# Performance work log

Measured on AMD Instinct MI355X. Metric: run time of the kernel, lower is better.

The kernel has to match this reference:

```python
import jax, jax.numpy as jnp
import numpy as np

EMBED_DIM = 1024
NUM_HEADS = 16
HEAD_DIM = EMBED_DIM // NUM_HEADS
B, S = 4, 2048


def setup_inputs() -> dict:
    key = jax.random.key(0)
    ks = jax.random.split(key, 9)
    scale = 1.0 / np.sqrt(EMBED_DIM)
    x = jax.random.normal(ks[0], (B, S, EMBED_DIM), dtype=jnp.float32)
    Wq = jax.random.uniform(ks[1], (EMBED_DIM, EMBED_DIM), jnp.float32, -scale, scale)
    bq = jax.random.uniform(ks[2], (EMBED_DIM,), jnp.float32, -scale, scale)
    Wk = jax.random.uniform(ks[3], (EMBED_DIM, EMBED_DIM), jnp.float32, -scale, scale)
    bk = jax.random.uniform(ks[4], (EMBED_DIM,), jnp.float32, -scale, scale)
    Wv = jax.random.uniform(ks[5], (EMBED_DIM, EMBED_DIM), jnp.float32, -scale, scale)
    bv = jax.random.uniform(ks[6], (EMBED_DIM,), jnp.float32, -scale, scale)
    Wo = jax.random.uniform(ks[7], (EMBED_DIM, EMBED_DIM), jnp.float32, -scale, scale)
    bo = jax.random.uniform(ks[8], (EMBED_DIM,), jnp.float32, -scale, scale)
    return {"x": x, "Wq": Wq, "bq": bq, "Wk": Wk, "bk": bk, "Wv": Wv, "bv": bv, "Wo": Wo, "bo": bo}


def reference(x, Wq, bq, Wk, bk, Wv, bv, Wo, bo):
    b, s, d = x.shape
    h, hd = NUM_HEADS, HEAD_DIM
    # projections -> [b, h, s, hd]
    def proj(W, bias):
        return (x @ W + bias).reshape(b, s, h, hd).transpose(0, 2, 1, 3)
    q = proj(Wq, bq)
    k = proj(Wk, bk)
    v = proj(Wv, bv)
    logits = jnp.einsum('bhqd,bhkd->bhqk', q, k) / np.sqrt(hd).astype(np.float32)
    attn = jax.nn.softmax(logits, axis=-1)  # dropout p=0.0 -> identity
    vals = jnp.einsum('bhqk,bhkd->bhqd', attn, v)
    vals = vals.transpose(0, 2, 1, 3).reshape(b, s, d)
    return vals @ Wo + bo
```

## Files before the change

kernel.cpp:

```cpp
#include <hip/hip_runtime.h>

typedef unsigned short u16;
typedef unsigned int u32;
typedef __bf16 bf16x8 __attribute__((ext_vector_type(8)));
typedef float f32x4 __attribute__((ext_vector_type(4)));
typedef float f32x16 __attribute__((ext_vector_type(16)));
typedef u32 u32x4 __attribute__((ext_vector_type(4)));
typedef u32 u32x2 __attribute__((ext_vector_type(2)));

#define NBATCH 4
#define NS 2048
#define ND 1024
#define NH 16
#define HDIM 64
#define KSCALE (0.125f * 1.44269504f)

#define MFMA(a, b, c) __builtin_amdgcn_mfma_f32_16x16x32_bf16(a, b, c, 0, 0, 0)
#define MFMA32(a, b, c) __builtin_amdgcn_mfma_f32_32x32x16_bf16(a, b, c, 0, 0, 0)

__device__ __forceinline__ u16 f2bf(float f) {
    u32 u = __builtin_bit_cast(u32, f);
    u += 0x7fffu + ((u >> 16) & 1u);
    return (u16)(u >> 16);
}

__device__ __forceinline__ u32 cvtpk(float a, float b) {
    u32 r;
    asm("v_cvt_pk_bf16_f32 %0, %1, %2" : "=v"(r) : "v"(a), "v"(b));
    return r;
}

__device__ __forceinline__ bf16x8 ldfrag(const u16* p) {
    u32x4 v = *(const u32x4*)p;
    return __builtin_bit_cast(bf16x8, v);
}

__device__ __forceinline__ void gld16(u16* lds, const u16* g) {
    __builtin_amdgcn_global_load_lds((__attribute__((address_space(1))) u32*)g,
                                     (__attribute__((address_space(3))) u32*)lds, 16, 0, 0);
}

__global__ __launch_bounds__(256) void cvt_f32_bf16(const float* __restrict__ src,
                                                    u16* __restrict__ dst) {
    const size_t i = ((size_t)blockIdx.x * 256 + threadIdx.x) * 4;
    float4 v = *(const float4*)(src + i);
    uint2 o;
    o.x = (u32)f2bf(v.x) | ((u32)f2bf(v.y) << 16);
    o.y = (u32)f2bf(v.z) | ((u32)f2bf(v.w) << 16);
    *(uint2*)(dst + i) = o;
}

__global__ __launch_bounds__(256) void wtrans4(const float* __restrict__ W0, const float* __restrict__ W1,
                                               const float* __restrict__ W2, const float* __restrict__ W3,
                                               u16* __restrict__ T0, u16* __restrict__ T1,
                                               u16* __restrict__ T2, u16* __restrict__ T3) {
    const int z = blockIdx.z;
    const float* W = z == 0 ? W0 : z == 1 ? W1 : z == 2 ? W2 : W3;
    u16* WT = z == 0 ? T0 : z == 1 ? T1 : z == 2 ? T2 : T3;
    __shared__ u16 t[64][72];
    const int tid = threadIdx.x;
    const int k0 = blockIdx.x * 64, n0 = blockIdx.y * 64;
    {
        const int r = tid >> 2, cq = (tid & 3) * 16;
#pragma unroll
        for (int i = 0; i < 4; ++i) {
            float4 v = *(const float4*)(W + (size_t)(k0 + r) * ND + n0 + cq + i * 4);
            t[r][cq + i * 4 + 0] = f2bf(v.x);
            t[r][cq + i * 4 + 1] = f2bf(v.y);
            t[r][cq + i * 4 + 2] = f2bf(v.z);
            t[r][cq + i * 4 + 3] = f2bf(v.w);
        }
    }
    __syncthreads();
    {
        const int rr = tid >> 2, cq = (tid & 3) * 16;
        u32x4 o0, o1;
#pragma unroll
        for (int j = 0; j < 4; ++j) {
            o0[j] = (u32)t[cq + 2 * j][rr] | ((u32)t[cq + 2 * j + 1][rr] << 16);
            o1[j] = (u32)t[cq + 8 + 2 * j][rr] | ((u32)t[cq + 8 + 2 * j + 1][rr] << 16);
        }
        u16* out = WT + (size_t)(n0 + rr) * ND + k0 + cq;
        *(u32x4*)out = o0;
        *(u32x4*)(out + 8) = o1;
    }
}

__global__ __launch_bounds__(256) void gemm_qkv(const u16* __restrict__ A,
                                                const u16* __restrict__ wqT, const u16* __restrict__ wkT,
                                                const u16* __restrict__ wvT,
                                                const float* __restrict__ bq, const float* __restrict__ bk,
                                                const float* __restrict__ bv,
                                                u16* __restrict__ Qp, u16* __restrict__ Kf,
                                                u16* __restrict__ Vf) {
    __shared__ u16 la[128 * 32];
    __shared__ u16 lb[128 * 32];
    const int wg = blockIdx.x;
    const int xcd = wg & 7, idx = wg >> 3;
    const int ybl = xcd * 8 + idx / 24;
    const int xbl = idx % 24;
    const int region = xbl >> 3;
    const int m0 = ybl * 128, n0 = (xbl & 7) * 128;
    const u16* Bt = region == 0 ? wqT : region == 1 ? wkT : wvT;
    const float* bias = region == 0 ? bq : region == 1 ? bk : bv;

    const int tid = threadIdx.x;
    const int l = tid & 63, w = tid >> 6;
    const int lr = l & 15, lg = l >> 4;
    const int wr = w >> 1, wc = w & 1;

    const int idx0 = tid, idx1 = tid + 256;
    const int row0 = idx0 >> 2, row1 = idx1 >> 2;
    const int sc0 = ((idx0 & 3) ^ ((row0 >> 1) & 3)) * 8;
    const int sc1 = ((idx1 & 3) ^ ((row1 >> 1) & 3)) * 8;
    const u16* Ar0 = A + (size_t)(m0 + row0) * ND + sc0;
    const u16* Ar1 = A + (size_t)(m0 + row1) * ND + sc1;
    const u16* Br0 = Bt + (size_t)(n0 + row0) * ND + sc0;
    const u16* Br1 = Bt + (size_t)(n0 + row1) * ND + sc1;

    f32x4 acc[4][4] = {};

    for (int kt = 0; kt < 32; ++kt) {
        const int k0 = kt * 32;
        __syncthreads();
        gld16(&la[idx0 * 8], Ar0 + k0);
        gld16(&la[idx1 * 8], Ar1 + k0);
        gld16(&lb[idx0 * 8], Br0 + k0);
        gld16(&lb[idx1 * 8], Br1 + k0);
        __syncthreads();

        bf16x8 af[4], bv4[4];
#pragma unroll
        for (int mb = 0; mb < 4; ++mb) {
            int row = wr * 64 + mb * 16 + lr;
            int off = row * 32 + (((lg * 16) ^ (((row >> 1) & 3) << 4)) >> 1);
            af[mb] = ldfrag(&la[off]);
        }
#pragma unroll
        for (int nb = 0; nb < 4; ++nb) {
            int row = wc * 64 + nb * 16 + lr;
            int off = row * 32 + (((lg * 16) ^ (((row >> 1) & 3) << 4)) >> 1);
            bv4[nb] = ldfrag(&lb[off]);
        }
#pragma unroll
        for (int mb = 0; mb < 4; ++mb)
#pragma unroll
            for (int nb = 0; nb < 4; ++nb)
                acc[mb][nb] = MFMA(af[mb], bv4[nb], acc[mb][nb]);
    }

#pragma unroll
    for (int mb = 0; mb < 4; ++mb) {
#pragma unroll
        for (int nb = 0; nb < 4; ++nb) {
            const int col = n0 + wc * 64 + nb * 16 + lr;
            const float bia = bias[col];
            const int hd = col & 63, h = col >> 6;
            if (region == 2) {
                const int rowb = m0 + wr * 64 + mb * 16 + lg * 4;
                const int b = rowb >> 11, kv = rowb & 2047;
                const int bh = b * NH + h;
                const int ktp = kv >> 6, ks = (kv >> 4) & 3, hif = (kv >> 3) & 1, j0 = kv & 7;
                const int lane = (hd & 31) | (hif << 5);
                u32x2 o;
                o[0] = (u32)f2bf(acc[mb][nb][0] + bia) | ((u32)f2bf(acc[mb][nb][1] + bia) << 16);
                o[1] = (u32)f2bf(acc[mb][nb][2] + bia) | ((u32)f2bf(acc[mb][nb][3] + bia) << 16);
                size_t off = (size_t)bh * 131072 + (size_t)ktp * 4096 +
                             (size_t)(((ks + 4 * (hd >> 5)) * 64 + lane) * 8 + j0);
                *(u32x2*)(Vf + off) = o;
            } else if (region == 1) {
#pragma unroll
                for (int r = 0; r < 4; ++r) {
                    const int rowg = m0 + wr * 64 + mb * 16 + lg * 4 + r;
                    float v = (acc[mb][nb][r] + bia) * KSCALE;
                    const int b = rowg >> 11, kv = rowg & 2047;
                    const int bh = b * NH + h;
                    const int ktp = kv >> 6, kvb = (kv >> 5) & 1;
                    const int lane = (kv & 31) | (((hd >> 3) & 1) << 5);
                    size_t o = (size_t)bh * 131072 + (size_t)ktp * 4096 +
                               (size_t)(((kvb * 4 + (hd >> 4)) * 64 + lane) * 8 + (hd & 7));
                    Kf[o] = f2bf(v);
                }
            } else {
#pragma unroll
                for (int r = 0; r < 4; ++r) {
                    const int rowg = m0 + wr * 64 + mb * 16 + lg * 4 + r;
                    float v = acc[mb][nb][r] + bia;
                    size_t o = ((size_t)((rowg >> 11) * NH + h) * NS + (rowg & 2047)) * HDIM + hd;
                    Qp[o] = f2bf(v);
                }
            }
        }
    }
}

__global__ __launch_bounds__(256) void gemm_o(const u16* __restrict__ A, const u16* __restrict__ Bt,
                                              const float* __restrict__ bias, float* __restrict__ of32) {
    __shared__ u16 la[128 * 32];
    __shared__ u16 lb[128 * 32];
    const int wg = blockIdx.x;
    const int xcd = wg & 7, idx = wg >> 3;
    const int ybl = xcd * 8 + (idx >> 3);
    const int xbl = idx & 7;
    const int m0 = ybl * 128, n0 = xbl * 128;

    const int tid = threadIdx.x;
    const int l = tid & 63, w = tid >> 6;
    const int lr = l & 15, lg = l >> 4;
    const int wr = w >> 1, wc = w & 1;

    const int idx0 = tid, idx1 = tid + 256;
    const int row0 = idx0 >> 2, row1 = idx1 >> 2;
    const int sc0 = ((idx0 & 3) ^ ((row0 >> 1) & 3)) * 8;
    const int sc1 = ((idx1 & 3) ^ ((row1 >> 1) & 3)) * 8;
    const u16* Ar0 = A + (size_t)(m0 + row0) * ND + sc0;
    const u16* Ar1 = A + (size_t)(m0 + row1) * ND + sc1;
    const u16* Br0 = Bt + (size_t)(n0 + row0) * ND + sc0;
    const u16* Br1 = Bt + (size_t)(n0 + row1) * ND + sc1;

    f32x4 acc[4][4] = {};

    for (int kt = 0; kt < 32; ++kt) {
        const int k0 = kt * 32;
        __syncthreads();
        gld16(&la[idx0 * 8], Ar0 + k0);
        gld16(&la[idx1 * 8], Ar1 + k0);
        gld16(&lb[idx0 * 8], Br0 + k0);
        gld16(&lb[idx1 * 8], Br1 + k0);
        __syncthreads();

        bf16x8 af[4], bv4[4];
#pragma unroll
        for (int mb = 0; mb < 4; ++mb) {
            int row = wr * 64 + mb * 16 + lr;
            int off = row * 32 + (((lg * 16) ^ (((row >> 1) & 3) << 4)) >> 1);
            af[mb] = ldfrag(&la[off]);
        }
#pragma unroll
        for (int nb = 0; nb < 4; ++nb) {
            int row = wc * 64 + nb * 16 + lr;
            int off = row * 32 + (((lg * 16) ^ (((row >> 1) & 3) << 4)) >> 1);
            bv4[nb] = ldfrag(&lb[off]);
        }
#pragma unroll
        for (int mb = 0; mb < 4; ++mb)
#pragma unroll
            for (int nb = 0; nb < 4; ++nb)
                acc[mb][nb] = MFMA(af[mb], bv4[nb], acc[mb][nb]);
    }

#pragma unroll
    for (int mb = 0; mb < 4; ++mb) {
#pragma unroll
        for (int nb = 0; nb < 4; ++nb) {
            const int col = n0 + wc * 64 + nb * 16 + lr;
            const float bia = bias[col];
#pragma unroll
            for (int r = 0; r < 4; ++r) {
                const int rowg = m0 + wr * 64 + mb * 16 + lg * 4 + r;
                of32[(size_t)rowg * ND + col] = acc[mb][nb][r] + bia;
            }
        }
    }
}

__global__ __launch_bounds__(256, 3) void attn(const u16* __restrict__ Q, const u16* __restrict__ Kf,
                                               const u16* __restrict__ Vf, u16* __restrict__ AO) {
    __shared__ u16 sm[16384];
    const int tid = threadIdx.x;
    const int l = tid & 63, w = tid >> 6;
    const int lq = l & 31, hi = l >> 5;
    const int wg = blockIdx.x;
    const int xcd = wg & 7, idx = wg >> 3;
    const int bh = xcd * 8 + (idx >> 4);
    const int qb = idx & 15;
    const int qbase = qb * 128 + w * 32;

    const u16* Qrow = Q + ((size_t)bh * NS + qbase + lq) * HDIM;
    bf16x8 qf[4];
#pragma unroll
    for (int kh = 0; kh < 4; ++kh) qf[kh] = ldfrag(Qrow + kh * 16 + hi * 8);

    f32x16 oacc[2] = {};
    float ls0 = 0.f, ls1 = 0.f, ls2 = 0.f, ls3 = 0.f;

    const u16* KfB = Kf + (size_t)bh * 131072;
    const u16* VfB = Vf + (size_t)bh * 131072;

    gld16(sm + tid * 8, KfB + tid * 8);
    gld16(sm + (256 + tid) * 8, KfB + (256 + tid) * 8);
    gld16(sm + 8192 + tid * 8, VfB + tid * 8);
    gld16(sm + 8192 + (256 + tid) * 8, VfB + (256 + tid) * 8);
    __syncthreads();

    for (int kt = 0; kt < 32; ++kt) {
        const int cur = kt & 1;
        if (kt < 31) {
            const u16* kg = KfB + (size_t)(kt + 1) * 4096;
            const u16* vg = VfB + (size_t)(kt + 1) * 4096;
            u16* kd = sm + (cur ^ 1) * 4096;
            u16* vd = sm + 8192 + (cur ^ 1) * 4096;
            gld16(kd + tid * 8, kg + tid * 8);
            gld16(kd + (256 + tid) * 8, kg + (256 + tid) * 8);
            gld16(vd + tid * 8, vg + tid * 8);
            gld16(vd + (256 + tid) * 8, vg + (256 + tid) * 8);
        }
        const u16* klb = sm + cur * 4096;
        const u16* vlb = sm + 8192 + cur * 4096;

        bf16x8 kf[2][4];
#pragma unroll
        for (int kvb = 0; kvb < 2; ++kvb)
#pragma unroll
            for (int kh = 0; kh < 4; ++kh)
                kf[kvb][kh] = ldfrag(klb + ((kvb * 4 + kh) * 64 + l) * 8);

        f32x16 sacc[2] = {};
        __builtin_amdgcn_s_setprio(1);
#pragma unroll
        for (int kvb = 0; kvb < 2; ++kvb)
#pragma unroll
            for (int kh = 0; kh < 4; ++kh)
                sacc[kvb] = MFMA32(kf[kvb][kh], qf[kh], sacc[kvb]);
        __builtin_amdgcn_s_setprio(0);

        bf16x8 vf[2][4];
#pragma unroll
        for (int hdb = 0; hdb < 2; ++hdb)
#pragma unroll
            for (int ks = 0; ks < 4; ++ks)
                vf[hdb][ks] = ldfrag(vlb + ((hdb * 4 + ks) * 64 + l) * 8);

#pragma unroll
        for (int kvb = 0; kvb < 2; ++kvb) {
#pragma unroll
            for (int i = 0; i < 16; i += 4) {
                float p0 = __builtin_amdgcn_exp2f(sacc[kvb][i + 0]);
                float p1 = __builtin_amdgcn_exp2f(sacc[kvb][i + 1]);
                float p2 = __builtin_amdgcn_exp2f(sacc[kvb][i + 2]);
                float p3 = __builtin_amdgcn_exp2f(sacc[kvb][i + 3]);
                sacc[kvb][i + 0] = p0;
                sacc[kvb][i + 1] = p1;
                sacc[kvb][i + 2] = p2;
                sacc[kvb][i + 3] = p3;
                ls0 += p0;
                ls1 += p1;
                ls2 += p2;
                ls3 += p3;
            }
        }

        bf16x8 pf[4];
#pragma unroll
        for (int ks = 0; ks < 4; ++ks) {
            const int i0 = 2 * ks, i1 = 2 * ks + 1;
            const int q20 = i0 & 3, kvb0 = i0 >> 2;
            const int q21 = i1 & 3, kvb1 = i1 >> 2;
            u32 W00 = cvtpk(sacc[kvb0][4 * q20 + 0], sacc[kvb0][4 * q20 + 1]);
            u32 W01 = cvtpk(sacc[kvb0][4 * q20 + 2], sacc[kvb0][4 * q20 + 3]);
            u32 W10 = cvtpk(sacc[kvb1][4 * q21 + 0], sacc[kvb1][4 * q21 + 1]);
            u32 W11 = cvtpk(sacc[kvb1][4 * q21 + 2], sacc[kvb1][4 * q21 + 3]);
            u32x2 s0 = __builtin_amdgcn_permlane32_swap(W00, W10, false, false);
            u32x2 s1 = __builtin_amdgcn_permlane32_swap(W01, W11, false, false);
            u32x4 words;
            words[0] = s0[0];
            words[1] = s1[0];
            words[2] = s0[1];
            words[3] = s1[1];
            pf[ks] = __builtin_bit_cast(bf16x8, words);
        }

        __builtin_amdgcn_s_setprio(1);
#pragma unroll
        for (int hdb = 0; hdb < 2; ++hdb)
#pragma unroll
            for (int ks = 0; ks < 4; ++ks)
                oacc[hdb] = MFMA32(vf[hdb][ks], pf[ks], oacc[hdb]);
        __builtin_amdgcn_s_setprio(0);

        __syncthreads();
    }

    float lsum = (ls0 + ls1) + (ls2 + ls3);
    lsum += __shfl_xor(lsum, 32);

    u16* ot = sm + w * 2048;
    const float inv = 1.f / lsum;
#pragma unroll
    for (int hdb = 0; hdb < 2; ++hdb)
#pragma unroll
        for (int q2 = 0; q2 < 4; ++q2)
#pragma unroll
            for (int rp = 0; rp < 2; ++rp) {
                u32 word = cvtpk(oacc[hdb][4 * q2 + 2 * rp] * inv, oacc[hdb][4 * q2 + 2 * rp + 1] * inv);
                const int hd0 = hdb * 32 + 8 * q2 + 4 * hi + 2 * rp;
                const int byteoff = lq * 128 + ((2 * hd0) ^ ((lq & 7) << 4));
                *(u32*)((char*)ot + byteoff) = word;
            }
    const int b = bh >> 4, h = bh & 15;
#pragma unroll
    for (int p = 0; p < 4; ++p) {
        const int pidx = p * 64 + l;
        const int row = pidx >> 3;
        const int cb = ((pidx & 7) * 16) ^ ((row & 7) << 4);
        u32x4 val = *(u32x4*)((char*)ot + row * 128 + cb);
        *(u32x4*)(AO + ((size_t)b * NS + qbase - w * 32 + w * 32 + row) * ND + h * 64 + (pidx & 7) * 8) = val;
    }
}

extern "C" void kernel_launch(void* const* d_in, const int* in_sizes, int n_in,
                              void* d_out, int out_size, void* d_ws, size_t ws_size,
                              hipStream_t stream) {
    const float* x = (const float*)d_in[0];
    const float* Wq = (const float*)d_in[1];
    const float* bq = (const float*)d_in[2];
    const float* Wk = (const float*)d_in[3];
    const float* bk = (const float*)d_in[4];
    const float* Wv = (const float*)d_in[5];
    const float* bv = (const float*)d_in[6];
    const float* Wo = (const float*)d_in[7];
    const float* bo = (const float*)d_in[8];
    float* out = (float*)d_out;

    u16* ws = (u16*)d_ws;
    u16* xb = ws;
    u16* wqT = ws + 8388608;
    u16* wkT = wqT + 1048576;
    u16* wvT = wkT + 1048576;
    u16* woT = wvT + 1048576;
    u16* Qp = woT + 1048576;
    u16* Kfp = Qp + 8388608;
    u16* Vfp = Kfp + 8388608;
    u16* AO = xb;

    cvt_f32_bf16<<<8192, 256, 0, stream>>>(x, xb);
    wtrans4<<<dim3(16, 16, 4), 256, 0, stream>>>(Wq, Wk, Wv, Wo, wqT, wkT, wvT, woT);
    gemm_qkv<<<1536, 256, 0, stream>>>(xb, wqT, wkT, wvT, bq, bk, bv, Qp, Kfp, Vfp);
    attn<<<1024, 256, 0, stream>>>(Qp, Kfp, Vfp, AO);
    gemm_o<<<512, 256, 0, stream>>>(AO, woT, bo, out);
}
```

Baseline: 197.3 us.

## Pre-tile GEMM operands into fragment order and double-buffer LDS loads

The bf16 conversion of x, the weight transpose and the attention output store now write operands in 128x32 tiles laid out in MFMA fragment order. Each GEMM tile load then becomes a contiguous 8KB copy, and fragment reads from LDS need no swizzle arithmetic. Both GEMMs double-buffer LDS so the next k-tile's global_load_lds overlaps the current MFMAs, with one barrier per iteration and raised wave priority around the MFMA block. The cost is twice the LDS per block, and producer kernels now write in a scattered pattern.

```diff
diff --git a/kernel.cpp b/kernel.cpp
--- a/kernel.cpp
+++ b/kernel.cpp
@@ -40,14 +40,28 @@
                                      (__attribute__((address_space(3))) u32*)lds, 16, 0, 0);
 }
 
-__global__ __launch_bounds__(256) void cvt_f32_bf16(const float* __restrict__ src,
-                                                    u16* __restrict__ dst) {
-    const size_t i = ((size_t)blockIdx.x * 256 + threadIdx.x) * 4;
-    float4 v = *(const float4*)(src + i);
-    uint2 o;
-    o.x = (u32)f2bf(v.x) | ((u32)f2bf(v.y) << 16);
-    o.y = (u32)f2bf(v.z) | ((u32)f2bf(v.w) << 16);
-    *(uint2*)(dst + i) = o;
+
+__global__ __launch_bounds__(256) void cvt_tile(const float* __restrict__ src, u16* __restrict__ dst) {
+    const int tile = blockIdx.x;
+    const int mt = tile >> 5, ktile = tile & 31;
+    const int tid = threadIdx.x;
+    u16* out = dst + (size_t)tile * 4096;
+#pragma unroll
+    for (int half = 0; half < 2; ++half) {
+        const int s = half * 256 + tid;
+        const int rg = s >> 6, l = s & 63;
+        const int row = mt * 128 + rg * 16 + (l & 15);
+        const int col = ktile * 32 + (l >> 4) * 8;
+        const float* sp = src + (size_t)row * ND + col;
+        float4 v0 = *(const float4*)sp;
+        float4 v1 = *(const float4*)(sp + 4);
+        u32x4 o;
+        o[0] = (u32)f2bf(v0.x) | ((u32)f2bf(v0.y) << 16);
+        o[1] = (u32)f2bf(v0.z) | ((u32)f2bf(v0.w) << 16);
+        o[2] = (u32)f2bf(v1.x) | ((u32)f2bf(v1.y) << 16);
+        o[3] = (u32)f2bf(v1.z) | ((u32)f2bf(v1.w) << 16);
+        *(u32x4*)(out + s * 8) = o;
+    }
 }
 
 __global__ __launch_bounds__(256) void wtrans4(const float* __restrict__ W0, const float* __restrict__ W1,
@@ -80,9 +94,13 @@
             o0[j] = (u32)t[cq + 2 * j][rr] | ((u32)t[cq + 2 * j + 1][rr] << 16);
             o1[j] = (u32)t[cq + 8 + 2 * j][rr] | ((u32)t[cq + 8 + 2 * j + 1][rr] << 16);
         }
-        u16* out = WT + (size_t)(n0 + rr) * ND + k0 + cq;
-        *(u32x4*)out = o0;
-        *(u32x4*)(out + 8) = o1;
+        const int n_g = n0 + rr;
+        const int nt = n_g >> 7, rgn = (n_g >> 4) & 7, lr = n_g & 15;
+        const int k_g = k0 + cq;
+        const int kt2 = k_g >> 5, lg = (k_g >> 3) & 3;
+        u16* outb = WT + ((size_t)(nt * 32 + kt2)) * 4096 + rgn * 512 + lr * 8;
+        *(u32x4*)(outb + lg * 128) = o0;
+        *(u32x4*)(outb + (lg + 1) * 128) = o1;
     }
 }
 
@@ -93,8 +111,8 @@
                                                 const float* __restrict__ bv,
                                                 u16* __restrict__ Qp, u16* __restrict__ Kf,
                                                 u16* __restrict__ Vf) {
-    __shared__ u16 la[128 * 32];
-    __shared__ u16 lb[128 * 32];
+    __shared__ u16 la[8192];
+    __shared__ u16 lb[8192];
     const int wg = blockIdx.x;
     const int xcd = wg & 7, idx = wg >> 3;
     const int ybl = xcd * 8 + idx / 24;
@@ -109,44 +127,47 @@
     const int lr = l & 15, lg = l >> 4;
     const int wr = w >> 1, wc = w & 1;
 
-    const int idx0 = tid, idx1 = tid + 256;
-    const int row0 = idx0 >> 2, row1 = idx1 >> 2;
-    const int sc0 = ((idx0 & 3) ^ ((row0 >> 1) & 3)) * 8;
-    const int sc1 = ((idx1 & 3) ^ ((row1 >> 1) & 3)) * 8;
-    const u16* Ar0 = A + (size_t)(m0 + row0) * ND + sc0;
-    const u16* Ar1 = A + (size_t)(m0 + row1) * ND + sc1;
-    const u16* Br0 = Bt + (size_t)(n0 + row0) * ND + sc0;
-    const u16* Br1 = Bt + (size_t)(n0 + row1) * ND + sc1;
+    const u16* Atiles = A + (size_t)ybl * 32 * 4096;
+    const u16* Btiles = Bt + (size_t)(xbl & 7) * 32 * 4096;
+
+    gld16(la + tid * 8, Atiles + tid * 8);
+    gld16(la + (256 + tid) * 8, Atiles + (256 + tid) * 8);
+    gld16(lb + tid * 8, Btiles + tid * 8);
+    gld16(lb + (256 + tid) * 8, Btiles + (256 + tid) * 8);
+    __syncthreads();
 
     f32x4 acc[4][4] = {};
 
     for (int kt = 0; kt < 32; ++kt) {
-        const int k0 = kt * 32;
-        __syncthreads();
-        gld16(&la[idx0 * 8], Ar0 + k0);
-        gld16(&la[idx1 * 8], Ar1 + k0);
-        gld16(&lb[idx0 * 8], Br0 + k0);
-        gld16(&lb[idx1 * 8], Br1 + k0);
-        __syncthreads();
+        const int cur = kt & 1;
+        if (kt < 31) {
+            const u16* ag = Atiles + (size_t)(kt + 1) * 4096;
+            const u16* bg = Btiles + (size_t)(kt + 1) * 4096;
+            u16* ad = la + (cur ^ 1) * 4096;
+            u16* bd = lb + (cur ^ 1) * 4096;
+            gld16(ad + tid * 8, ag + tid * 8);
+            gld16(ad + (256 + tid) * 8, ag + (256 + tid) * 8);
+            gld16(bd + tid * 8, bg + tid * 8);
+            gld16(bd + (256 + tid) * 8, bg + (256 + tid) * 8);
+        }
+        const u16* al = la + cur * 4096;
+        const u16* bl = lb + cur * 4096;
 
         bf16x8 af[4], bv4[4];
 #pragma unroll
-        for (int mb = 0; mb < 4; ++mb) {
-            int row = wr * 64 + mb * 16 + lr;
-            int off = row * 32 + (((lg * 16) ^ (((row >> 1) & 3) << 4)) >> 1);
-            af[mb] = ldfrag(&la[off]);
-        }
-#pragma unroll
-        for (int nb = 0; nb < 4; ++nb) {
-            int row = wc * 64 + nb * 16 + lr;
-            int off = row * 32 + (((lg * 16) ^ (((row >> 1) & 3) << 4)) >> 1);
-            bv4[nb] = ldfrag(&lb[off]);
-        }
+        for (int mb = 0; mb < 4; ++mb) af[mb] = ldfrag(al + ((wr * 4 + mb) * 64 + l) * 8);
+#pragma unroll
+        for (int nb = 0; nb < 4; ++nb) bv4[nb] = ldfrag(bl + ((wc * 4 + nb) * 64 + l) * 8);
+
+        __builtin_amdgcn_s_setprio(1);
 #pragma unroll
         for (int mb = 0; mb < 4; ++mb)
 #pragma unroll
             for (int nb = 0; nb < 4; ++nb)
                 acc[mb][nb] = MFMA(af[mb], bv4[nb], acc[mb][nb]);
+        __builtin_amdgcn_s_setprio(0);
+
+        __syncthreads();
     }
 
 #pragma unroll
@@ -196,8 +217,8 @@
 
 __global__ __launch_bounds__(256) void gemm_o(const u16* __restrict__ A, const u16* __restrict__ Bt,
                                               const float* __restrict__ bias, float* __restrict__ of32) {
-    __shared__ u16 la[128 * 32];
-    __shared__ u16 lb[128 * 32];
+    __shared__ u16 la[8192];
+    __shared__ u16 lb[8192];
     const int wg = blockIdx.x;
     const int xcd = wg & 7, idx = wg >> 3;
     const int ybl = xcd * 8 + (idx >> 3);
@@ -209,44 +230,47 @@
     const int lr = l & 15, lg = l >> 4;
     const int wr = w >> 1, wc = w & 1;
 
-    const int idx0 = tid, idx1 = tid + 256;
-    const int row0 = idx0 >> 2, row1 = idx1 >> 2;
-    const int sc0 = ((idx0 & 3) ^ ((row0 >> 1) & 3)) * 8;
-    const int sc1 = ((idx1 & 3) ^ ((row1 >> 1) & 3)) * 8;
-    const u16* Ar0 = A + (size_t)(m0 + row0) * ND + sc0;
-    const u16* Ar1 = A + (size_t)(m0 + row1) * ND + sc1;
-    const u16* Br0 = Bt + (size_t)(n0 + row0) * ND + sc0;
-    const u16* Br1 = Bt + (size_t)(n0 + row1) * ND + sc1;
+    const u16* Atiles = A + (size_t)ybl * 32 * 4096;
+    const u16* Btiles = Bt + (size_t)xbl * 32 * 4096;
+
+    gld16(la + tid * 8, Atiles + tid * 8);
+    gld16(la + (256 + tid) * 8, Atiles + (256 + tid) * 8);
+    gld16(lb + tid * 8, Btiles + tid * 8);
+    gld16(lb + (256 + tid) * 8, Btiles + (256 + tid) * 8);
+    __syncthreads();
 
     f32x4 acc[4][4] = {};
 
     for (int kt = 0; kt < 32; ++kt) {
-        const int k0 = kt * 32;
-        __syncthreads();
-        gld16(&la[idx0 * 8], Ar0 + k0);
-        gld16(&la[idx1 * 8], Ar1 + k0);
-        gld16(&lb[idx0 * 8], Br0 + k0);
-        gld16(&lb[idx1 * 8], Br1 + k0);
-        __syncthreads();
+        const int cur = kt & 1;
+        if (kt < 31) {
+            const u16* ag = Atiles + (size_t)(kt + 1) * 4096;
+            const u16* bg = Btiles + (size_t)(kt + 1) * 4096;
+            u16* ad = la + (cur ^ 1) * 4096;
+            u16* bd = lb + (cur ^ 1) * 4096;
+            gld16(ad + tid * 8, ag + tid * 8);
+            gld16(ad + (256 + tid) * 8, ag + (256 + tid) * 8);
+            gld16(bd + tid * 8, bg + tid * 8);
+            gld16(bd + (256 + tid) * 8, bg + (256 + tid) * 8);
+        }
+        const u16* al = la + cur * 4096;
+        const u16* bl = lb + cur * 4096;
 
         bf16x8 af[4], bv4[4];
 #pragma unroll
-        for (int mb = 0; mb < 4; ++mb) {
-            int row = wr * 64 + mb * 16 + lr;
-            int off = row * 32 + (((lg * 16) ^ (((row >> 1) & 3) << 4)) >> 1);
-            af[mb] = ldfrag(&la[off]);
-        }
-#pragma unroll
-        for (int nb = 0; nb < 4; ++nb) {
-            int row = wc * 64 + nb * 16 + lr;
-            int off = row * 32 + (((lg * 16) ^ (((row >> 1) & 3) << 4)) >> 1);
-            bv4[nb] = ldfrag(&lb[off]);
-        }
+        for (int mb = 0; mb < 4; ++mb) af[mb] = ldfrag(al + ((wr * 4 + mb) * 64 + l) * 8);
+#pragma unroll
+        for (int nb = 0; nb < 4; ++nb) bv4[nb] = ldfrag(bl + ((wc * 4 + nb) * 64 + l) * 8);
+
+        __builtin_amdgcn_s_setprio(1);
 #pragma unroll
         for (int mb = 0; mb < 4; ++mb)
 #pragma unroll
             for (int nb = 0; nb < 4; ++nb)
                 acc[mb][nb] = MFMA(af[mb], bv4[nb], acc[mb][nb]);
+        __builtin_amdgcn_s_setprio(0);
+
+        __syncthreads();
     }
 
 #pragma unroll
@@ -404,7 +428,11 @@
         const int row = pidx >> 3;
         const int cb = ((pidx & 7) * 16) ^ ((row & 7) << 4);
         u32x4 val = *(u32x4*)((char*)ot + row * 128 + cb);
-        *(u32x4*)(AO + ((size_t)b * NS + qbase - w * 32 + w * 32 + row) * ND + h * 64 + (pidx & 7) * 8) = val;
+        const int m = b * NS + qbase + row;
+        const int c = h * 64 + (pidx & 7) * 8;
+        const int mt = m >> 7, rg = (m >> 4) & 7, lrm = m & 15;
+        const int ktile = c >> 5, lgc = (c >> 3) & 3;
+        *(u32x4*)(AO + ((size_t)(mt * 32 + ktile)) * 4096 + rg * 512 + (lgc * 16 + lrm) * 8) = val;
     }
 }
 
@@ -433,7 +461,7 @@
     u16* Vfp = Kfp + 8388608;
     u16* AO = xb;
 
-    cvt_f32_bf16<<<8192, 256, 0, stream>>>(x, xb);
+    cvt_tile<<<2048, 256, 0, stream>>>(x, xb);
     wtrans4<<<dim3(16, 16, 4), 256, 0, stream>>>(Wq, Wk, Wv, Wo, wqT, wkT, wvT, woT);
     gemm_qkv<<<1536, 256, 0, stream>>>(xb, wqT, wkT, wvT, bq, bk, bv, Qp, Kfp, Vfp);
     attn<<<1024, 256, 0, stream>>>(Qp, Kfp, Vfp, AO);
```

Measured after the change: 201.5 us. 2.1% more time.
